# Optimization experiments

Hardware: AMD Instinct MI355X
Metric: run time of the kernel (lower is better)

The kernel has to match this reference:

```python
import jax, jax.numpy as jnp
import numpy as np

B, P, S, H, R = 32, 512, 1024, 1024, 256


def setup_inputs() -> dict:
    key = jax.random.key(0)
    k1, k2, k3 = jax.random.split(key, 3)
    pairs = jax.random.randint(k1, (B, P, 2, 2), 0, S, dtype=jnp.int64 if jax.config.jax_enable_x64 else jnp.int32)
    hidden_states = jax.random.normal(k2, (B, S, H), dtype=jnp.float32)
    W = jax.random.normal(k3, (R, 3 * H), dtype=jnp.float32) * (1.0 / np.sqrt(3 * H))
    b = jnp.zeros((R,), dtype=jnp.float32)
    return {"pairs": pairs, "hidden_states": hidden_states, "W": W, "b": b}


def reference(pairs, hidden_states, W, b):
    # pairs: [B, P, 2, 2] -> [:, :, 0, :] = (h_start, h_end), [:, :, 1, :] = (t_start, t_end)
    def gather_tokens(idx):  # idx: [B, P] -> [B, P, H]
        return jnp.take_along_axis(hidden_states, idx[:, :, None], axis=1)

    head_embed = 0.5 * (gather_tokens(pairs[:, :, 0, 0]) + gather_tokens(pairs[:, :, 0, 1]))
    tail_embed = 0.5 * (gather_tokens(pairs[:, :, 1, 0]) + gather_tokens(pairs[:, :, 1, 1]))
    feats = jnp.concatenate([head_embed, tail_embed, head_embed * tail_embed], axis=-1)  # [B, P, 3H]
    logits = jnp.einsum('bpf,rf->bpr', feats, W) + b  # [B, P, R]
    return logits
```

## Files before the change

kernel.cpp:

```cpp
#include <hip/hip_runtime.h>

#define NB 32
#define NP 512
#define NS 1024
#define NH 1024
#define NR 256
#define K3 3072

#define BM 64
#define BK 64
#define KP 72

typedef short short8 __attribute__((ext_vector_type(8)));
typedef short short4v __attribute__((ext_vector_type(4)));
typedef __bf16 bf16x8 __attribute__((ext_vector_type(8)));
typedef float f32x4 __attribute__((ext_vector_type(4)));

__device__ __forceinline__ unsigned short f2bf(float f) {
  unsigned u = __builtin_bit_cast(unsigned, f);
  u += 0x7fffu + ((u >> 16) & 1u);
  return (unsigned short)(u >> 16);
}

__device__ __forceinline__ f32x4 mfma_bf16(short8 a, short8 b, f32x4 c) {
  return __builtin_amdgcn_mfma_f32_16x16x32_bf16(
      __builtin_bit_cast(bf16x8, a), __builtin_bit_cast(bf16x8, b), c, 0, 0, 0);
}

__global__ void wconv_kernel(const float* __restrict__ W,
                             unsigned short* __restrict__ WbF) {
  int i = blockIdx.x * blockDim.x + threadIdx.x;
  int lane = i & 63, n16 = (i >> 6) & 15, kc = i >> 10;
  int lr = lane & 15, lg = lane >> 4;
  const float* src = W + (size_t)(n16 * 16 + lr) * K3 + kc * 32 + lg * 8;
  float4 a = *(const float4*)src;
  float4 b = *(const float4*)(src + 4);
  short8 o;
  o[0] = (short)f2bf(a.x); o[1] = (short)f2bf(a.y);
  o[2] = (short)f2bf(a.z); o[3] = (short)f2bf(a.w);
  o[4] = (short)f2bf(b.x); o[5] = (short)f2bf(b.y);
  o[6] = (short)f2bf(b.z); o[7] = (short)f2bf(b.w);
  *(short8*)(WbF + (size_t)i * 8) = o;
}

__global__ __launch_bounds__(512, 2) void gemm_kernel(
    const int* __restrict__ pairs, const float* __restrict__ hs,
    const unsigned short* __restrict__ WbF, const float* __restrict__ bias,
    float* __restrict__ out) {
  __shared__ __align__(16) unsigned short sA[2][3][BM][KP];

  const int tid = threadIdx.x;
  const int blk = blockIdx.x;
  const int x     = blk & 7;
  const int jb    = blk >> 3;
  const int batch = x * 4 + (jb >> 3);
  const int mtile = jb & 7;
  const int m0    = (batch * 8 + mtile) * BM;

  const int pairi = tid >> 3;
  const int q     = tid & 7;
  int4 pr = ((const int4*)pairs)[m0 + pairi];
  const float* hb = hs + (size_t)batch * NS * NH;
  const float* rp[4];
  rp[0] = hb + (size_t)pr.x * NH + 4 * q;
  rp[1] = hb + (size_t)pr.y * NH + 4 * q;
  rp[2] = hb + (size_t)pr.z * NH + 4 * q;
  rp[3] = hb + (size_t)pr.w * NH + 4 * q;

  const int lane = tid & 63;
  const int w    = tid >> 6;
  const int lr   = lane & 15;
  const int lg   = lane >> 4;

  const unsigned short* wb = WbF + (size_t)(w * 2) * 512 + (size_t)lane * 8;

  f32x4 acc[4][2];
#pragma unroll
  for (int i = 0; i < 4; ++i)
#pragma unroll
    for (int j = 0; j < 2; ++j) acc[i][j] = (f32x4){0.f, 0.f, 0.f, 0.f};

  float4 ld[8];

  auto load_stage = [&](int s) {
    const int o = s * BK;
#pragma unroll
    for (int jj = 0; jj < 8; ++jj)
      ld[jj] = *(const float4*)(rp[jj >> 1] + o + 32 * (jj & 1));
  };

  auto store_stage = [&](int buf) {
#pragma unroll
    for (int c = 0; c < 2; ++c) {
      short4v hv, tv, pv;
#pragma unroll
      for (int e = 0; e < 4; ++e) {
        float h = 0.5f * (((const float*)&ld[0 + c])[e] + ((const float*)&ld[2 + c])[e]);
        float t = 0.5f * (((const float*)&ld[4 + c])[e] + ((const float*)&ld[6 + c])[e]);
        float p = h * t;
        hv[e] = (short)f2bf(h); tv[e] = (short)f2bf(t); pv[e] = (short)f2bf(p);
      }
      const int c0 = 4 * q + 32 * c;
      *(short4v*)&sA[buf][0][pairi][c0] = hv;
      *(short4v*)&sA[buf][1][pairi][c0] = tv;
      *(short4v*)&sA[buf][2][pairi][c0] = pv;
    }
  };

  load_stage(0);
  store_stage(0);

  for (int s = 0; s < 16; ++s) {
    __syncthreads();
    const int buf = s & 1;
    if (s < 15) load_stage(s + 1);

#pragma unroll
    for (int ks = 0; ks < 2; ++ks) {
      const int koff = ks * 32 + lg * 8;
      short8 ah[4], at4[4], ap[4];
#pragma unroll
      for (int i = 0; i < 4; ++i) {
        ah[i]  = *(const short8*)&sA[buf][0][i * 16 + lr][koff];
        at4[i] = *(const short8*)&sA[buf][1][i * 16 + lr][koff];
        ap[i]  = *(const short8*)&sA[buf][2][i * 16 + lr][koff];
      }
#pragma unroll
      for (int j = 0; j < 2; ++j) {
        const unsigned short* wp = wb + (size_t)(s * 2 + ks) * 8192 + (size_t)j * 512;
        short8 b0 = *(const short8*)(wp);
        short8 b1 = *(const short8*)(wp + 32 * 8192);
        short8 b2 = *(const short8*)(wp + 64 * 8192);
#pragma unroll
        for (int i = 0; i < 4; ++i) {
          acc[i][j] = mfma_bf16(ah[i],  b0, acc[i][j]);
          acc[i][j] = mfma_bf16(at4[i], b1, acc[i][j]);
          acc[i][j] = mfma_bf16(ap[i],  b2, acc[i][j]);
        }
      }
    }
    if (s < 15) store_stage(buf ^ 1);
  }

#pragma unroll
  for (int j = 0; j < 2; ++j) {
    const int col  = w * 32 + j * 16 + lr;
    const float bv = bias[col];
#pragma unroll
    for (int i = 0; i < 4; ++i) {
      const size_t rbase = (size_t)(m0 + i * 16 + lg * 4) * NR + col;
#pragma unroll
      for (int r = 0; r < 4; ++r)
        out[rbase + (size_t)r * NR] = acc[i][j][r] + bv;
    }
  }
}

extern "C" void kernel_launch(void* const* d_in, const int* in_sizes, int n_in,
                              void* d_out, int out_size, void* d_ws, size_t ws_size,
                              hipStream_t stream) {
  const int*   pairs = (const int*)d_in[0];
  const float* hs    = (const float*)d_in[1];
  const float* W     = (const float*)d_in[2];
  const float* bias  = (const float*)d_in[3];
  float* out = (float*)d_out;
  unsigned short* WbF = (unsigned short*)d_ws;

  wconv_kernel<<<(96 * 16 * 64) / 256, 256, 0, stream>>>(W, WbF);
  gemm_kernel<<<(NB * NP) / BM, 512, 0, stream>>>(pairs, hs, WbF, bias, out);
}
```

Baseline: 239.4 us.

## Prefetch W fragments one stage ahead and XOR-swizzle shared A tiles

W fragments for the next K stage are now loaded into a second set of registers alongside the hidden-state gather, so the MFMA loop no longer stalls on global W loads inside the compute. The padded shared-memory layout for A is replaced by an XOR-swizzled unpadded layout to avoid LDS bank conflicts while cutting LDS footprint. The extra 24 short8 registers per thread raise register pressure at 512 threads with 2 blocks per CU, which may force spills or lower occupancy.

```diff
diff --git a/kernel.cpp b/kernel.cpp
--- a/kernel.cpp
+++ b/kernel.cpp
@@ -9,7 +9,6 @@
 
 #define BM 64
 #define BK 64
-#define KP 72
 
 typedef short short8 __attribute__((ext_vector_type(8)));
 typedef short short4v __attribute__((ext_vector_type(4)));
@@ -47,7 +46,7 @@
     const int* __restrict__ pairs, const float* __restrict__ hs,
     const unsigned short* __restrict__ WbF, const float* __restrict__ bias,
     float* __restrict__ out) {
-  __shared__ __align__(16) unsigned short sA[2][3][BM][KP];
+  __shared__ __align__(16) unsigned short sA[2][3][BM][64];
 
   const int tid = threadIdx.x;
   const int blk = blockIdx.x;
@@ -72,7 +71,7 @@
   const int lr   = lane & 15;
   const int lg   = lane >> 4;
 
-  const unsigned short* wb = WbF + (size_t)(w * 2) * 512 + (size_t)lane * 8;
+  const unsigned short* wbase = WbF + (size_t)(w * 2) * 512 + (size_t)lane * 8;
 
   f32x4 acc[4][2];
 #pragma unroll
@@ -81,8 +80,20 @@
     for (int j = 0; j < 2; ++j) acc[i][j] = (f32x4){0.f, 0.f, 0.f, 0.f};
 
   float4 ld[8];
+  short8 wcur[12], wnxt[12];
 
-  auto load_stage = [&](int s) {
+  auto load_w = [&](int s, short8* wd) {
+#pragma unroll
+    for (int part = 0; part < 3; ++part)
+#pragma unroll
+      for (int ks = 0; ks < 2; ++ks)
+#pragma unroll
+        for (int j = 0; j < 2; ++j)
+          wd[part * 4 + ks * 2 + j] = *(const short8*)(
+              wbase + (size_t)(part * 32 + s * 2 + ks) * 8192 + (size_t)j * 512);
+  };
+
+  auto load_gather = [&](int s) {
     const int o = s * BK;
 #pragma unroll
     for (int jj = 0; jj < 8; ++jj)
@@ -100,46 +111,55 @@
         float p = h * t;
         hv[e] = (short)f2bf(h); tv[e] = (short)f2bf(t); pv[e] = (short)f2bf(p);
       }
-      const int c0 = 4 * q + 32 * c;
-      *(short4v*)&sA[buf][0][pairi][c0] = hv;
-      *(short4v*)&sA[buf][1][pairi][c0] = tv;
-      *(short4v*)&sA[buf][2][pairi][c0] = pv;
+      const int chunkI = (q >> 1) + 4 * c;
+      const int col = ((chunkI ^ (pairi & 7)) * 8) + (q & 1) * 4;
+      *(short4v*)&sA[buf][0][pairi][col] = hv;
+      *(short4v*)&sA[buf][1][pairi][col] = tv;
+      *(short4v*)&sA[buf][2][pairi][col] = pv;
     }
   };
 
-  load_stage(0);
+  auto compute = [&](int buf, short8* wc) {
+#pragma unroll
+    for (int ks = 0; ks < 2; ++ks) {
+      short8 ah[4], at4[4], ap[4];
+      const int col = (((ks * 4 + lg) ^ (lr & 7)) * 8);
+#pragma unroll
+      for (int i = 0; i < 4; ++i) {
+        ah[i]  = *(const short8*)&sA[buf][0][i * 16 + lr][col];
+        at4[i] = *(const short8*)&sA[buf][1][i * 16 + lr][col];
+        ap[i]  = *(const short8*)&sA[buf][2][i * 16 + lr][col];
+      }
+#pragma unroll
+      for (int j = 0; j < 2; ++j)
+#pragma unroll
+        for (int i = 0; i < 4; ++i) {
+          acc[i][j] = mfma_bf16(ah[i],  wc[0 + ks * 2 + j], acc[i][j]);
+          acc[i][j] = mfma_bf16(at4[i], wc[4 + ks * 2 + j], acc[i][j]);
+          acc[i][j] = mfma_bf16(ap[i],  wc[8 + ks * 2 + j], acc[i][j]);
+        }
+    }
+  };
+
+  load_w(0, wcur);
+  load_gather(0);
   store_stage(0);
 
-  for (int s = 0; s < 16; ++s) {
+  auto stage = [&](int s, short8* wc, short8* wn) {
     __syncthreads();
     const int buf = s & 1;
-    if (s < 15) load_stage(s + 1);
+    if (s < 15) {
+      load_w(s + 1, wn);
+      load_gather(s + 1);
+    }
+    compute(buf, wc);
+    if (s < 15) store_stage(buf ^ 1);
+  };
 
-#pragma unroll
-    for (int ks = 0; ks < 2; ++ks) {
-      const int koff = ks * 32 + lg * 8;
-      short8 ah[4], at4[4], ap[4];
-#pragma unroll
-      for (int i = 0; i < 4; ++i) {
-        ah[i]  = *(const short8*)&sA[buf][0][i * 16 + lr][koff];
-        at4[i] = *(const short8*)&sA[buf][1][i * 16 + lr][koff];
-        ap[i]  = *(const short8*)&sA[buf][2][i * 16 + lr][koff];
-      }
-#pragma unroll
-      for (int j = 0; j < 2; ++j) {
-        const unsigned short* wp = wb + (size_t)(s * 2 + ks) * 8192 + (size_t)j * 512;
-        short8 b0 = *(const short8*)(wp);
-        short8 b1 = *(const short8*)(wp + 32 * 8192);
-        short8 b2 = *(const short8*)(wp + 64 * 8192);
-#pragma unroll
-        for (int i = 0; i < 4; ++i) {
-          acc[i][j] = mfma_bf16(ah[i],  b0, acc[i][j]);
-          acc[i][j] = mfma_bf16(at4[i], b1, acc[i][j]);
-          acc[i][j] = mfma_bf16(ap[i],  b2, acc[i][j]);
-        }
-      }
-    }
-    if (s < 15) store_stage(buf ^ 1);
+#pragma unroll 1
+  for (int sp = 0; sp < 8; ++sp) {
+    stage(2 * sp,     wcur, wnxt);
+    stage(2 * sp + 1, wnxt, wcur);
   }
 
 #pragma unroll
```

New measurement: 232.0 us. -3.1%, faster.
